# Kernel tuning notes

Measured on AMD Instinct MI355X. Metric: run time of the kernel, lower is better.

## Reference

```python
import jax, jax.numpy as jnp
import numpy as np

B_, T_, L_, M_, H_, F_ = 16, 2048, 128, 256, 512, 1024
EPS = 1e-5


def _init_reservoir(h, rng):
    # orthogonal matrix scaled inside the unit disk for a stable linear recurrence
    q, _ = np.linalg.qr(rng.standard_normal((h, h)).astype(np.float32))
    return jnp.asarray(0.95 * q, dtype=jnp.float32)


def setup_inputs() -> dict:
    key = jax.random.key(0)
    ks = jax.random.split(key, 8)
    rng = np.random.default_rng(0)
    s = lambda fan_in: 1.0 / np.sqrt(fan_in)
    return {
        "x": jax.random.normal(ks[0], (B_, T_, L_), dtype=jnp.float32),
        "We": jax.random.uniform(ks[1], (L_, M_), jnp.float32, -s(L_), s(L_)),
        "be": jnp.zeros((M_,), jnp.float32),
        "Wb": jax.random.uniform(ks[2], (M_, H_), jnp.float32, -s(M_), s(M_)),
        "A": _init_reservoir(H_, rng),
        "Wr": jax.random.uniform(ks[3], (L_, H_), jnp.float32, -s(L_), s(L_)),
        "br": jnp.zeros((H_,), jnp.float32),
        "ln_g": jnp.ones((H_,), jnp.float32),
        "ln_b": jnp.zeros((H_,), jnp.float32),
        "W1": jax.random.uniform(ks[4], (H_, F_), jnp.float32, -s(H_), s(H_)),
        "b1": jnp.zeros((F_,), jnp.float32),
        "W2": jax.random.uniform(ks[5], (F_, H_), jnp.float32, -s(F_), s(F_)),
        "b2": jnp.zeros((H_,), jnp.float32),
    }


def reference(x, We, be, Wb, A, Wr, br, ln_g, ln_b, W1, b1, W2, b2):
    # encoder + B projection, batched over all timesteps: [B,T,H]
    Bu = (x @ We + be) @ Wb

    # sequential linear recurrence h_t = h_{t-1} @ A + Bu_t, h_0 = Bu_0
    def step(h, bu_t):
        h = h @ A + bu_t
        return h, h

    h0 = jnp.zeros((x.shape[0], A.shape[0]), x.dtype)
    _, Hs = jax.lax.scan(step, h0, jnp.swapaxes(Bu, 0, 1))  # [T,B,H]
    H_seq = jnp.swapaxes(Hs, 0, 1)  # [B,T,H]

    # residual + layer norm
    z = H_seq + (x @ Wr + br)
    mu = jnp.mean(z, axis=-1, keepdims=True)
    var = jnp.mean(jnp.square(z - mu), axis=-1, keepdims=True)
    zn = (z - mu) * jax.lax.rsqrt(var + EPS) * ln_g + ln_b

    # MLP on last timestep
    h_last = zn[:, -1, :]
    out = jax.nn.relu(h_last @ W1 + b1) @ W2 + b2
    return out
```

## Files before the change

### kernel.cpp

```cpp
#include <hip/hip_runtime.h>

#define B_  16
#define T_  2048
#define L_  128
#define M_  256
#define H_  512
#define F_  1024
#define EPS 1e-5f

#define LDA_S 36
#define LDB_S 68
#define SMSZ (64 * LDA_S + 64 * LDB_S)

__device__ __forceinline__ float4 load_a4(const float* __restrict__ A,
                                          const float* __restrict__ Alast,
                                          int M, int lda, int amode,
                                          int gr, int gk) {
    float4 av = make_float4(0.f, 0.f, 0.f, 0.f);
    if (gr < M) {
        const float* p;
        if (amode == 1)
            p = A + (long)((gr & 15) * T_ + (T_ - 1 - (gr >> 4))) * L_ + gk;
        else if (amode == 2)
            p = A + (long)(((gr >> 4) << 5) + 16 + (gr & 15)) * lda + gk;
        else if (amode == 3 && gr == M - 1)
            p = Alast + gk;
        else
            p = A + (long)gr * lda + gk;
        av = *(const float4*)p;
    }
    return av;
}

__device__ __forceinline__ void gemm_tile(
    float* sm,
    const float* __restrict__ A, const float* __restrict__ Alast,
    const float* __restrict__ Bm, const float* __restrict__ bias,
    const float* __restrict__ Add, float* __restrict__ C,
    int M, int K, int lda, int ldb, int ldc,
    int flags, int amode, int bx, int by)
{
    constexpr int BM = 32, BN = 64, BK = 64, TM = 2, TN = 4;
    float* As = sm;
    float* Bs = sm + BK * LDA_S;
    const int tid = threadIdx.x;
    const int tx = tid & 15;
    const int ty = tid >> 4;
    const int row0 = by * BM, col0 = bx * BN;

    float4 pa[2], pb[4];
#pragma unroll
    for (int t = 0; t < 2; ++t) {
        int f = tid + t * 256;
        pa[t] = load_a4(A, Alast, M, lda, amode, row0 + (f >> 4), (f & 15) * 4);
    }
#pragma unroll
    for (int t = 0; t < 4; ++t) {
        int f = tid + t * 256;
        pb[t] = *(const float4*)(Bm + (long)(f >> 4) * ldb + col0 + (f & 15) * 4);
    }

    float acc[TM][TN] = {};

    for (int k0 = 0; k0 < K; k0 += BK) {
        __syncthreads();
#pragma unroll
        for (int t = 0; t < 2; ++t) {
            int f = tid + t * 256;
            int arow = f >> 4, kk = (f & 15) * 4;
            As[(kk + 0) * LDA_S + arow] = pa[t].x;
            As[(kk + 1) * LDA_S + arow] = pa[t].y;
            As[(kk + 2) * LDA_S + arow] = pa[t].z;
            As[(kk + 3) * LDA_S + arow] = pa[t].w;
        }
#pragma unroll
        for (int t = 0; t < 4; ++t) {
            int f = tid + t * 256;
            *(float4*)&Bs[(f >> 4) * LDB_S + (f & 15) * 4] = pb[t];
        }
        __syncthreads();
        int kn = k0 + BK;
        if (kn < K) {
#pragma unroll
            for (int t = 0; t < 2; ++t) {
                int f = tid + t * 256;
                pa[t] = load_a4(A, Alast, M, lda, amode, row0 + (f >> 4), kn + (f & 15) * 4);
            }
#pragma unroll
            for (int t = 0; t < 4; ++t) {
                int f = tid + t * 256;
                pb[t] = *(const float4*)(Bm + (long)(kn + (f >> 4)) * ldb + col0 + (f & 15) * 4);
            }
        }
#pragma unroll
        for (int kk = 0; kk < BK; ++kk) {
            float ra[TM], rb[TN];
#pragma unroll
            for (int i = 0; i < TM; ++i) ra[i] = As[kk * LDA_S + ty * TM + i];
#pragma unroll
            for (int j = 0; j < TN; ++j) rb[j] = Bs[kk * LDB_S + tx * TN + j];
#pragma unroll
            for (int i = 0; i < TM; ++i)
#pragma unroll
                for (int j = 0; j < TN; ++j)
                    acc[i][j] = fmaf(ra[i], rb[j], acc[i][j]);
        }
    }

#pragma unroll
    for (int i = 0; i < TM; ++i) {
        int r = row0 + ty * TM + i;
        if (r >= M) continue;
#pragma unroll
        for (int j = 0; j < TN; ++j) {
            int c = col0 + tx * TN + j;
            float v = acc[i][j];
            if (flags & 1) v += bias[c];
            if (amode == 2) v += Add[(long)(((r >> 4) << 5) + (r & 15)) * ldc + c];
            C[(long)r * ldc + c] = v;
        }
    }
}

__global__ __launch_bounds__(256) void dual(
    const float* A, const float* Alast, const float* Bm, const float* bias,
    const float* Add, float* C, int M, int K, int lda, int ldb, int ldc,
    int flags, int amode, int nbxA, int nA,
    const float* SqL, const float* SqR, float* SqOut)
{
    __shared__ float sm[SMSZ];
    int j = blockIdx.x;
    if (j < nA)
        gemm_tile(sm, A, Alast, Bm, bias, Add, C, M, K, lda, ldb, ldc,
                  flags, amode, j % nbxA, j / nbxA);
    else {
        int s = j - nA;
        gemm_tile(sm, SqL, nullptr, SqR, nullptr, nullptr, SqOut,
                  H_, H_, H_, H_, H_, 0, 0, s % 8, s / 8);
    }
}

#define TLDA 20
#define TLDB 68
#define TSM (64 * TLDA + 64 * TLDB)

template <int MODE>
__device__ __forceinline__ float4 tail_a4(const float* __restrict__ Asrc,
                                          const float* __restrict__ x,
                                          int b, int gk) {
    if (MODE == 0) {
        int seg = gk >> 9;
        if (seg < 3)
            return *(const float4*)(Asrc + (long)((seg + 1) * 16 + b) * H_ + (gk & 511));
        return *(const float4*)(x + ((long)b * T_ + (T_ - 1)) * L_ + (gk - 1536));
    } else if (MODE == 1) {
        return *(const float4*)(Asrc + (long)b * H_ + gk);
    } else {
        return *(const float4*)(Asrc + (long)b * F_ + gk);
    }
}

template <int MODE>
__device__ __forceinline__ float4 tail_b4(const float* __restrict__ P32,
                                          const float* __restrict__ P64,
                                          const float* __restrict__ P96,
                                          const float* __restrict__ WrB,
                                          int kr, int c) {
    if (MODE == 0) {
        const float* p;
        if (kr < 512)       p = P32 + (long)kr * H_;
        else if (kr < 1024) p = P64 + (long)(kr - 512) * H_;
        else if (kr < 1536) p = P96 + (long)(kr - 1024) * H_;
        else                p = WrB + (long)(kr - 1536) * H_;
        return *(const float4*)(p + c);
    } else if (MODE == 1) {
        return *(const float4*)(WrB + (long)kr * F_ + c);
    } else {
        return *(const float4*)(WrB + (long)kr * H_ + c);
    }
}

template <int MODE>
__global__ __launch_bounds__(256) void tailgemm(
    const float* __restrict__ Asrc, const float* __restrict__ x,
    const float* __restrict__ P32, const float* __restrict__ P64,
    const float* __restrict__ P96, const float* __restrict__ WrB,
    float* __restrict__ parts, int nbx, int kLen)
{
    constexpr int LDC = (MODE == 1) ? F_ : H_;
    __shared__ float sm[TSM];
    float* As = sm;
    float* Bs = sm + 64 * TLDA;
    const int tid = threadIdx.x;
    const int tx = tid & 15, ty = tid >> 4;
    const int kc = blockIdx.x / nbx;
    const int col0 = (blockIdx.x % nbx) * 64;
    const int kOff = kc * kLen;

    float4 pa, pb[4];
    {
        int gk = kOff + (tid & 15) * 4;
        pa = tail_a4<MODE>(Asrc, x, tid >> 4, gk);
#pragma unroll
        for (int t = 0; t < 4; ++t) {
            int f = tid + t * 256;
            pb[t] = tail_b4<MODE>(P32, P64, P96, WrB, kOff + (f >> 4), col0 + (f & 15) * 4);
        }
    }

    float acc[4] = {};
    for (int k0 = kOff; k0 < kOff + kLen; k0 += 64) {
        __syncthreads();
        {
            int arow = tid >> 4, kk = (tid & 15) * 4;
            As[(kk + 0) * TLDA + arow] = pa.x;
            As[(kk + 1) * TLDA + arow] = pa.y;
            As[(kk + 2) * TLDA + arow] = pa.z;
            As[(kk + 3) * TLDA + arow] = pa.w;
        }
#pragma unroll
        for (int t = 0; t < 4; ++t) {
            int f = tid + t * 256;
            *(float4*)&Bs[(f >> 4) * TLDB + (f & 15) * 4] = pb[t];
        }
        __syncthreads();
        int kn = k0 + 64;
        if (kn < kOff + kLen) {
            pa = tail_a4<MODE>(Asrc, x, tid >> 4, kn + (tid & 15) * 4);
#pragma unroll
            for (int t = 0; t < 4; ++t) {
                int f = tid + t * 256;
                pb[t] = tail_b4<MODE>(P32, P64, P96, WrB, kn + (f >> 4), col0 + (f & 15) * 4);
            }
        }
#pragma unroll
        for (int kk = 0; kk < 64; ++kk) {
            float ra = As[kk * TLDA + ty];
            float4 rb = *(float4*)&Bs[kk * TLDB + tx * 4];
            acc[0] = fmaf(ra, rb.x, acc[0]);
            acc[1] = fmaf(ra, rb.y, acc[1]);
            acc[2] = fmaf(ra, rb.z, acc[2]);
            acc[3] = fmaf(ra, rb.w, acc[3]);
        }
    }

    float* dst = parts + (long)kc * 16 * LDC + (long)ty * LDC + col0 + tx * 4;
    *(float4*)dst = make_float4(acc[0], acc[1], acc[2], acc[3]);
}

__global__ __launch_bounds__(256) void zlnred(
    const float* __restrict__ V1, const float* __restrict__ zparts,
    const float* __restrict__ br, const float* __restrict__ lng,
    const float* __restrict__ lnb, float* __restrict__ zn)
{
    __shared__ float red1[4], red2[4];
    const int b = blockIdx.x, tid = threadIdx.x;
    float z[2];
#pragma unroll
    for (int jj = 0; jj < 2; ++jj) {
        int c = tid + jj * 256;
        float s = V1[(long)b * H_ + c] + br[c];
#pragma unroll
        for (int kc = 0; kc < 13; ++kc)
            s += zparts[(long)kc * 16 * H_ + (long)b * H_ + c];
        z[jj] = s;
    }
    float s1 = z[0] + z[1];
    float s2 = z[0] * z[0] + z[1] * z[1];
#pragma unroll
    for (int off = 32; off > 0; off >>= 1) {
        s1 += __shfl_down(s1, off, 64);
        s2 += __shfl_down(s2, off, 64);
    }
    int wid = tid >> 6, lane = tid & 63;
    if (lane == 0) { red1[wid] = s1; red2[wid] = s2; }
    __syncthreads();
    float S1 = red1[0] + red1[1] + red1[2] + red1[3];
    float S2 = red2[0] + red2[1] + red2[2] + red2[3];
    float mu  = S1 * (1.0f / H_);
    float var = S2 * (1.0f / H_) - mu * mu;
    float rs  = rsqrtf(var + EPS);
#pragma unroll
    for (int jj = 0; jj < 2; ++jj) {
        int c = tid + jj * 256;
        zn[(long)b * H_ + c] = (z[jj] - mu) * rs * lng[c] + lnb[c];
    }
}

__global__ __launch_bounds__(256) void hred(
    const float* __restrict__ h1p, const float* __restrict__ b1,
    float* __restrict__ hid)
{
    int b = blockIdx.x >> 2;
    int c = (blockIdx.x & 3) * 256 + threadIdx.x;
    float s = b1[c];
#pragma unroll
    for (int kc = 0; kc < 4; ++kc)
        s += h1p[(long)kc * 16 * F_ + (long)b * F_ + c];
    hid[(long)b * F_ + c] = fmaxf(s, 0.f);
}

__global__ __launch_bounds__(256) void ored(
    const float* __restrict__ op, const float* __restrict__ b2,
    float* __restrict__ out)
{
    int b = blockIdx.x >> 1;
    int c = (blockIdx.x & 1) * 256 + threadIdx.x;
    float s = b2[c];
#pragma unroll
    for (int kc = 0; kc < 8; ++kc)
        s += op[(long)kc * 16 * H_ + (long)b * H_ + c];
    out[(long)b * H_ + c] = s;
}

extern "C" void kernel_launch(void* const* d_in, const int* in_sizes, int n_in,
                              void* d_out, int out_size, void* d_ws, size_t ws_size,
                              hipStream_t stream) {
    const float* x    = (const float*)d_in[0];
    const float* We   = (const float*)d_in[1];
    const float* be   = (const float*)d_in[2];
    const float* Wb   = (const float*)d_in[3];
    const float* Amat = (const float*)d_in[4];
    const float* Wr   = (const float*)d_in[5];
    const float* br   = (const float*)d_in[6];
    const float* lng  = (const float*)d_in[7];
    const float* lnb  = (const float*)d_in[8];
    const float* W1   = (const float*)d_in[9];
    const float* b1   = (const float*)d_in[10];
    const float* W2   = (const float*)d_in[11];
    const float* b2   = (const float*)d_in[12];
    float* out = (float*)d_out;

    float* ws  = (float*)d_ws;
    float* Wc  = ws;
    float* V0  = Wc + 129 * H_;
    float* V1  = V0 + 2048 * H_;
    float* P2  = V1 + 1024 * H_;
    float* P4  = P2 + H_ * H_;
    float* P8  = P4 + H_ * H_;
    float* P16 = P8 + H_ * H_;
    float* P32 = P16 + H_ * H_;
    float* P64 = P32 + H_ * H_;
    float* P96 = P64 + H_ * H_;
    float* zn  = P96 + H_ * H_;
    float* hid = zn + B_ * H_;
    float* zp  = hid + B_ * F_;
    float* h1p = zp + 13 * B_ * H_;
    float* op  = h1p + 4 * B_ * F_;

    dual<<<168, 256, 0, stream>>>(We, be, Wb, nullptr, nullptr, Wc,
                                  129, M_, M_, H_, H_, 0, 3, 8, 40,
                                  Amat, Amat, P2);
    dual<<<640, 256, 0, stream>>>(x, nullptr, Wc, Wc + 128 * H_, nullptr, V0,
                                  2048, L_, L_, H_, H_, 1, 1, 8, 512,
                                  P2, P2, P4);
    dual<<<384, 256, 0, stream>>>(V0, nullptr, Amat, nullptr, V0, V1,
                                  1024, H_, H_, H_, H_, 0, 2, 8, 256,
                                  P4, P4, P8);
    dual<<<256, 256, 0, stream>>>(V1, nullptr, P2, nullptr, V1, V0,
                                  512, H_, H_, H_, H_, 0, 2, 8, 128,
                                  P8, P8, P16);
    dual<<<192, 256, 0, stream>>>(V0, nullptr, P4, nullptr, V0, V1,
                                  256, H_, H_, H_, H_, 0, 2, 8, 64,
                                  P16, P16, P32);
    dual<<<160, 256, 0, stream>>>(V1, nullptr, P8, nullptr, V1, V0,
                                  128, H_, H_, H_, H_, 0, 2, 8, 32,
                                  P32, P32, P64);
    dual<<<144, 256, 0, stream>>>(V0, nullptr, P16, nullptr, V0, V1,
                                  64, H_, H_, H_, H_, 0, 2, 8, 16,
                                  P32, P64, P96);
    tailgemm<0><<<104, 256, 0, stream>>>(V1, x, P32, P64, P96, Wr, zp, 8, 128);
    zlnred<<<16, 256, 0, stream>>>(V1, zp, br, lng, lnb, zn);
    tailgemm<1><<<64, 256, 0, stream>>>(zn, nullptr, nullptr, nullptr, nullptr,
                                        W1, h1p, 16, 128);
    hred<<<64, 256, 0, stream>>>(h1p, b1, hid);
    tailgemm<2><<<64, 256, 0, stream>>>(hid, nullptr, nullptr, nullptr, nullptr,
                                        W2, op, 8, 128);
    ored<<<32, 256, 0, stream>>>(op, b2, out);
}
```

Before: 284.8 us.

## Use 128x128 split-K GEMM tiles with atomic accumulation and drop reduction kernels

Replaces the 32x64 GEMM tiles in the scan-doubling stages with 128x128 tiles using 8x8 per-thread micro-tiles, splitting K into 128-chunks whose partials are combined with atomicAdd. The tail GEMMs also accumulate atomically, and the hred/ored reduction kernels are removed, with bias and ReLU folded into the A-load of the last GEMM. The aim is more register reuse per loaded element and fewer launches. In exchange it adds a zeroing kernel over the whole workspace and the output, atomic traffic, nondeterministic summation order, and fewer blocks in the small stages.

```diff
diff --git a/kernel.cpp b/kernel.cpp
--- a/kernel.cpp
+++ b/kernel.cpp
@@ -8,135 +8,124 @@
 #define F_  1024
 #define EPS 1e-5f
 
-#define LDA_S 36
-#define LDB_S 68
-#define SMSZ (64 * LDA_S + 64 * LDB_S)
-
-__device__ __forceinline__ float4 load_a4(const float* __restrict__ A,
-                                          const float* __restrict__ Alast,
-                                          int M, int lda, int amode,
-                                          int gr, int gk) {
-    float4 av = make_float4(0.f, 0.f, 0.f, 0.f);
-    if (gr < M) {
-        const float* p;
-        if (amode == 1)
-            p = A + (long)((gr & 15) * T_ + (T_ - 1 - (gr >> 4))) * L_ + gk;
-        else if (amode == 2)
-            p = A + (long)(((gr >> 4) << 5) + 16 + (gr & 15)) * lda + gk;
-        else if (amode == 3 && gr == M - 1)
-            p = Alast + gk;
-        else
-            p = A + (long)gr * lda + gk;
-        av = *(const float4*)p;
-    }
-    return av;
-}
-
-__device__ __forceinline__ void gemm_tile(
+#define LDS_P 132
+#define SM128 (32 * LDS_P * 2)
+
+__device__ __forceinline__ float4 a_load(const float* __restrict__ A,
+                                         const float* __restrict__ Aaux,
+                                         int M, int lda, int amode,
+                                         int gr, int gk) {
+    if (gr >= M) return make_float4(0.f, 0.f, 0.f, 0.f);
+    const float* p;
+    if (amode == 1)
+        p = A + (long)((gr & 15) * T_ + (T_ - 1 - (gr >> 4))) * L_ + gk;
+    else if (amode == 2)
+        p = A + (long)(((gr >> 4) << 5) + 16 + (gr & 15)) * lda + gk;
+    else if (amode == 3 && gr == M - 1)
+        p = Aaux + gk;
+    else
+        p = A + (long)gr * lda + gk;
+    return *(const float4*)p;
+}
+
+__device__ __forceinline__ void gemm128(
     float* sm,
-    const float* __restrict__ A, const float* __restrict__ Alast,
-    const float* __restrict__ Bm, const float* __restrict__ bias,
+    const float* __restrict__ A, const float* __restrict__ Aaux,
+    const float* __restrict__ B, const float* __restrict__ bias,
     const float* __restrict__ Add, float* __restrict__ C,
-    int M, int K, int lda, int ldb, int ldc,
-    int flags, int amode, int bx, int by)
-{
-    constexpr int BM = 32, BN = 64, BK = 64, TM = 2, TN = 4;
+    int M, int lda, int kOff, int kLen, int amode, int kc, int bx, int by)
+{
     float* As = sm;
-    float* Bs = sm + BK * LDA_S;
+    float* Bs = sm + 32 * LDS_P;
     const int tid = threadIdx.x;
-    const int tx = tid & 15;
-    const int ty = tid >> 4;
-    const int row0 = by * BM, col0 = bx * BN;
-
-    float4 pa[2], pb[4];
-#pragma unroll
-    for (int t = 0; t < 2; ++t) {
-        int f = tid + t * 256;
-        pa[t] = load_a4(A, Alast, M, lda, amode, row0 + (f >> 4), (f & 15) * 4);
-    }
+    const int tx = tid & 15, ty = tid >> 4;
+    const int row0 = by * 128, col0 = bx * 128;
+
+    float4 pa[4], pb[4];
 #pragma unroll
     for (int t = 0; t < 4; ++t) {
         int f = tid + t * 256;
-        pb[t] = *(const float4*)(Bm + (long)(f >> 4) * ldb + col0 + (f & 15) * 4);
-    }
-
-    float acc[TM][TN] = {};
-
-    for (int k0 = 0; k0 < K; k0 += BK) {
+        pa[t] = a_load(A, Aaux, M, lda, amode, row0 + (f >> 3), kOff + (f & 7) * 4);
+        pb[t] = *(const float4*)(B + (long)(kOff + (f >> 5)) * H_ + col0 + (f & 31) * 4);
+    }
+
+    float acc[8][8] = {};
+
+    for (int k0 = 0; k0 < kLen; k0 += 32) {
         __syncthreads();
-#pragma unroll
-        for (int t = 0; t < 2; ++t) {
-            int f = tid + t * 256;
-            int arow = f >> 4, kk = (f & 15) * 4;
-            As[(kk + 0) * LDA_S + arow] = pa[t].x;
-            As[(kk + 1) * LDA_S + arow] = pa[t].y;
-            As[(kk + 2) * LDA_S + arow] = pa[t].z;
-            As[(kk + 3) * LDA_S + arow] = pa[t].w;
-        }
 #pragma unroll
         for (int t = 0; t < 4; ++t) {
             int f = tid + t * 256;
-            *(float4*)&Bs[(f >> 4) * LDB_S + (f & 15) * 4] = pb[t];
+            int ar = f >> 3, ak = (f & 7) * 4;
+            As[(ak + 0) * LDS_P + ar] = pa[t].x;
+            As[(ak + 1) * LDS_P + ar] = pa[t].y;
+            As[(ak + 2) * LDS_P + ar] = pa[t].z;
+            As[(ak + 3) * LDS_P + ar] = pa[t].w;
+            *(float4*)&Bs[(f >> 5) * LDS_P + (f & 31) * 4] = pb[t];
         }
         __syncthreads();
-        int kn = k0 + BK;
-        if (kn < K) {
-#pragma unroll
-            for (int t = 0; t < 2; ++t) {
-                int f = tid + t * 256;
-                pa[t] = load_a4(A, Alast, M, lda, amode, row0 + (f >> 4), kn + (f & 15) * 4);
-            }
+        int kn = k0 + 32;
+        if (kn < kLen) {
 #pragma unroll
             for (int t = 0; t < 4; ++t) {
                 int f = tid + t * 256;
-                pb[t] = *(const float4*)(Bm + (long)(kn + (f >> 4)) * ldb + col0 + (f & 15) * 4);
+                pa[t] = a_load(A, Aaux, M, lda, amode, row0 + (f >> 3),
+                               kOff + kn + (f & 7) * 4);
+                pb[t] = *(const float4*)(B + (long)(kOff + kn + (f >> 5)) * H_ +
+                                         col0 + (f & 31) * 4);
             }
         }
 #pragma unroll
-        for (int kk = 0; kk < BK; ++kk) {
-            float ra[TM], rb[TN];
-#pragma unroll
-            for (int i = 0; i < TM; ++i) ra[i] = As[kk * LDA_S + ty * TM + i];
-#pragma unroll
-            for (int j = 0; j < TN; ++j) rb[j] = Bs[kk * LDB_S + tx * TN + j];
-#pragma unroll
-            for (int i = 0; i < TM; ++i)
-#pragma unroll
-                for (int j = 0; j < TN; ++j)
+        for (int kk = 0; kk < 32; ++kk) {
+            float ra[8], rb[8];
+#pragma unroll
+            for (int i = 0; i < 8; ++i) ra[i] = As[kk * LDS_P + ty * 8 + i];
+#pragma unroll
+            for (int j = 0; j < 8; ++j) rb[j] = Bs[kk * LDS_P + tx * 8 + j];
+#pragma unroll
+            for (int i = 0; i < 8; ++i)
+#pragma unroll
+                for (int j = 0; j < 8; ++j)
                     acc[i][j] = fmaf(ra[i], rb[j], acc[i][j]);
         }
     }
 
 #pragma unroll
-    for (int i = 0; i < TM; ++i) {
-        int r = row0 + ty * TM + i;
+    for (int i = 0; i < 8; ++i) {
+        int r = row0 + ty * 8 + i;
         if (r >= M) continue;
-#pragma unroll
-        for (int j = 0; j < TN; ++j) {
-            int c = col0 + tx * TN + j;
+        long addoff = (amode == 2) ? (long)(((r >> 4) << 5) + (r & 15)) * H_ : 0;
+#pragma unroll
+        for (int j = 0; j < 8; ++j) {
+            int c = col0 + tx * 8 + j;
             float v = acc[i][j];
-            if (flags & 1) v += bias[c];
-            if (amode == 2) v += Add[(long)(((r >> 4) << 5) + (r & 15)) * ldc + c];
-            C[(long)r * ldc + c] = v;
-        }
-    }
-}
-
-__global__ __launch_bounds__(256) void dual(
-    const float* A, const float* Alast, const float* Bm, const float* bias,
-    const float* Add, float* C, int M, int K, int lda, int ldb, int ldc,
-    int flags, int amode, int nbxA, int nA,
-    const float* SqL, const float* SqR, float* SqOut)
-{
-    __shared__ float sm[SMSZ];
+            if (kc == 0 && bias) v += bias[c];
+            if (kc == 0 && Add)  v += Add[addoff + c];
+            atomicAdd(&C[(long)r * H_ + c], v);
+        }
+    }
+}
+
+__global__ __launch_bounds__(256) void dual128(
+    const float* A, const float* Aaux, const float* B, const float* bias,
+    const float* Add, float* C, int M, int lda, int kLen,
+    int nbxA, int nrtA, int amode, int nA,
+    const float* PL, const float* PR, float* PO)
+{
+    __shared__ float sm[SM128];
     int j = blockIdx.x;
-    if (j < nA)
-        gemm_tile(sm, A, Alast, Bm, bias, Add, C, M, K, lda, ldb, ldc,
-                  flags, amode, j % nbxA, j / nbxA);
-    else {
+    if (j < nA) {
+        int bx = j % nbxA;
+        int r  = j / nbxA;
+        int by = r % nrtA;
+        int kc = r / nrtA;
+        gemm128(sm, A, Aaux, B, bias, Add, C, M, lda, kc * kLen, kLen,
+                amode, kc, bx, by);
+    } else {
         int s = j - nA;
-        gemm_tile(sm, SqL, nullptr, SqR, nullptr, nullptr, SqOut,
-                  H_, H_, H_, H_, H_, 0, 0, s % 8, s / 8);
+        int bx = s & 3, by = (s >> 2) & 3, kc = s >> 4;
+        gemm128(sm, PL, nullptr, PR, nullptr, nullptr, PO, 512, 512,
+                kc * 128, 128, 0, kc, bx, by);
     }
 }
 
@@ -146,17 +135,20 @@
 
 template <int MODE>
 __device__ __forceinline__ float4 tail_a4(const float* __restrict__ Asrc,
-                                          const float* __restrict__ x,
+                                          const float* __restrict__ aux,
                                           int b, int gk) {
     if (MODE == 0) {
         int seg = gk >> 9;
         if (seg < 3)
             return *(const float4*)(Asrc + (long)((seg + 1) * 16 + b) * H_ + (gk & 511));
-        return *(const float4*)(x + ((long)b * T_ + (T_ - 1)) * L_ + (gk - 1536));
+        return *(const float4*)(aux + ((long)b * T_ + (T_ - 1)) * L_ + (gk - 1536));
     } else if (MODE == 1) {
         return *(const float4*)(Asrc + (long)b * H_ + gk);
     } else {
-        return *(const float4*)(Asrc + (long)b * F_ + gk);
+        float4 h = *(const float4*)(Asrc + (long)b * F_ + gk);
+        float4 bb = *(const float4*)(aux + gk);
+        return make_float4(fmaxf(h.x + bb.x, 0.f), fmaxf(h.y + bb.y, 0.f),
+                           fmaxf(h.z + bb.z, 0.f), fmaxf(h.w + bb.w, 0.f));
     }
 }
 
@@ -164,28 +156,29 @@
 __device__ __forceinline__ float4 tail_b4(const float* __restrict__ P32,
                                           const float* __restrict__ P64,
                                           const float* __restrict__ P96,
-                                          const float* __restrict__ WrB,
+                                          const float* __restrict__ WB,
                                           int kr, int c) {
     if (MODE == 0) {
         const float* p;
         if (kr < 512)       p = P32 + (long)kr * H_;
         else if (kr < 1024) p = P64 + (long)(kr - 512) * H_;
         else if (kr < 1536) p = P96 + (long)(kr - 1024) * H_;
-        else                p = WrB + (long)(kr - 1536) * H_;
+        else                p = WB + (long)(kr - 1536) * H_;
         return *(const float4*)(p + c);
     } else if (MODE == 1) {
-        return *(const float4*)(WrB + (long)kr * F_ + c);
+        return *(const float4*)(WB + (long)kr * F_ + c);
     } else {
-        return *(const float4*)(WrB + (long)kr * H_ + c);
+        return *(const float4*)(WB + (long)kr * H_ + c);
     }
 }
 
 template <int MODE>
 __global__ __launch_bounds__(256) void tailgemm(
-    const float* __restrict__ Asrc, const float* __restrict__ x,
+    const float* __restrict__ Asrc, const float* __restrict__ aux,
     const float* __restrict__ P32, const float* __restrict__ P64,
-    const float* __restrict__ P96, const float* __restrict__ WrB,
-    float* __restrict__ parts, int nbx, int kLen)
+    const float* __restrict__ P96, const float* __restrict__ WB,
+    const float* __restrict__ bias2, float* __restrict__ Cacc,
+    int nbx, int kLen)
 {
     constexpr int LDC = (MODE == 1) ? F_ : H_;
     __shared__ float sm[TSM];
@@ -198,25 +191,22 @@
     const int kOff = kc * kLen;
 
     float4 pa, pb[4];
-    {
-        int gk = kOff + (tid & 15) * 4;
-        pa = tail_a4<MODE>(Asrc, x, tid >> 4, gk);
-#pragma unroll
-        for (int t = 0; t < 4; ++t) {
-            int f = tid + t * 256;
-            pb[t] = tail_b4<MODE>(P32, P64, P96, WrB, kOff + (f >> 4), col0 + (f & 15) * 4);
-        }
+    pa = tail_a4<MODE>(Asrc, aux, ty, kOff + tx * 4);
+#pragma unroll
+    for (int t = 0; t < 4; ++t) {
+        int f = tid + t * 256;
+        pb[t] = tail_b4<MODE>(P32, P64, P96, WB, kOff + (f >> 4), col0 + (f & 15) * 4);
     }
 
     float acc[4] = {};
-    for (int k0 = kOff; k0 < kOff + kLen; k0 += 64) {
+    for (int k0 = 0; k0 < kLen; k0 += 64) {
         __syncthreads();
         {
-            int arow = tid >> 4, kk = (tid & 15) * 4;
-            As[(kk + 0) * TLDA + arow] = pa.x;
-            As[(kk + 1) * TLDA + arow] = pa.y;
-            As[(kk + 2) * TLDA + arow] = pa.z;
-            As[(kk + 3) * TLDA + arow] = pa.w;
+            int kk = tx * 4;
+            As[(kk + 0) * TLDA + ty] = pa.x;
+            As[(kk + 1) * TLDA + ty] = pa.y;
+            As[(kk + 2) * TLDA + ty] = pa.z;
+            As[(kk + 3) * TLDA + ty] = pa.w;
         }
 #pragma unroll
         for (int t = 0; t < 4; ++t) {
@@ -225,12 +215,13 @@
         }
         __syncthreads();
         int kn = k0 + 64;
-        if (kn < kOff + kLen) {
-            pa = tail_a4<MODE>(Asrc, x, tid >> 4, kn + (tid & 15) * 4);
+        if (kn < kLen) {
+            pa = tail_a4<MODE>(Asrc, aux, ty, kOff + kn + tx * 4);
 #pragma unroll
             for (int t = 0; t < 4; ++t) {
                 int f = tid + t * 256;
-                pb[t] = tail_b4<MODE>(P32, P64, P96, WrB, kn + (f >> 4), col0 + (f & 15) * 4);
+                pb[t] = tail_b4<MODE>(P32, P64, P96, WB, kOff + kn + (f >> 4),
+                                      col0 + (f & 15) * 4);
             }
         }
 #pragma unroll
@@ -244,12 +235,17 @@
         }
     }
 
-    float* dst = parts + (long)kc * 16 * LDC + (long)ty * LDC + col0 + tx * 4;
-    *(float4*)dst = make_float4(acc[0], acc[1], acc[2], acc[3]);
+    float* dst = Cacc + (long)ty * LDC + col0 + tx * 4;
+#pragma unroll
+    for (int q = 0; q < 4; ++q) {
+        float v = acc[q];
+        if (MODE == 2 && kc == 0 && bias2) v += bias2[col0 + tx * 4 + q];
+        atomicAdd(dst + q, v);
+    }
 }
 
 __global__ __launch_bounds__(256) void zlnred(
-    const float* __restrict__ V1, const float* __restrict__ zparts,
+    const float* __restrict__ Y5, const float* __restrict__ zacc,
     const float* __restrict__ br, const float* __restrict__ lng,
     const float* __restrict__ lnb, float* __restrict__ zn)
 {
@@ -259,11 +255,7 @@
 #pragma unroll
     for (int jj = 0; jj < 2; ++jj) {
         int c = tid + jj * 256;
-        float s = V1[(long)b * H_ + c] + br[c];
-#pragma unroll
-        for (int kc = 0; kc < 13; ++kc)
-            s += zparts[(long)kc * 16 * H_ + (long)b * H_ + c];
-        z[jj] = s;
+        z[jj] = Y5[(long)b * H_ + c] + zacc[(long)b * H_ + c] + br[c];
     }
     float s1 = z[0] + z[1];
     float s2 = z[0] * z[0] + z[1] * z[1];
@@ -287,30 +279,13 @@
     }
 }
 
-__global__ __launch_bounds__(256) void hred(
-    const float* __restrict__ h1p, const float* __restrict__ b1,
-    float* __restrict__ hid)
-{
-    int b = blockIdx.x >> 2;
-    int c = (blockIdx.x & 3) * 256 + threadIdx.x;
-    float s = b1[c];
-#pragma unroll
-    for (int kc = 0; kc < 4; ++kc)
-        s += h1p[(long)kc * 16 * F_ + (long)b * F_ + c];
-    hid[(long)b * F_ + c] = fmaxf(s, 0.f);
-}
-
-__global__ __launch_bounds__(256) void ored(
-    const float* __restrict__ op, const float* __restrict__ b2,
-    float* __restrict__ out)
-{
-    int b = blockIdx.x >> 1;
-    int c = (blockIdx.x & 1) * 256 + threadIdx.x;
-    float s = b2[c];
-#pragma unroll
-    for (int kc = 0; kc < 8; ++kc)
-        s += op[(long)kc * 16 * H_ + (long)b * H_ + c];
-    out[(long)b * H_ + c] = s;
+__global__ __launch_bounds__(256) void zerok(float4* w, long n4, float4* o, long n4o)
+{
+    long stride = (long)gridDim.x * 256;
+    for (long i = (long)blockIdx.x * 256 + threadIdx.x; i < n4; i += stride)
+        w[i] = make_float4(0.f, 0.f, 0.f, 0.f);
+    for (long i = (long)blockIdx.x * 256 + threadIdx.x; i < n4o; i += stride)
+        o[i] = make_float4(0.f, 0.f, 0.f, 0.f);
 }
 
 extern "C" void kernel_launch(void* const* d_in, const int* in_sizes, int n_in,
@@ -331,50 +306,47 @@
     const float* b2   = (const float*)d_in[12];
     float* out = (float*)d_out;
 
-    float* ws  = (float*)d_ws;
-    float* Wc  = ws;
-    float* V0  = Wc + 129 * H_;
-    float* V1  = V0 + 2048 * H_;
-    float* P2  = V1 + 1024 * H_;
-    float* P4  = P2 + H_ * H_;
-    float* P8  = P4 + H_ * H_;
-    float* P16 = P8 + H_ * H_;
-    float* P32 = P16 + H_ * H_;
-    float* P64 = P32 + H_ * H_;
-    float* P96 = P64 + H_ * H_;
-    float* zn  = P96 + H_ * H_;
-    float* hid = zn + B_ * H_;
-    float* zp  = hid + B_ * F_;
-    float* h1p = zp + 13 * B_ * H_;
-    float* op  = h1p + 4 * B_ * F_;
-
-    dual<<<168, 256, 0, stream>>>(We, be, Wb, nullptr, nullptr, Wc,
-                                  129, M_, M_, H_, H_, 0, 3, 8, 40,
-                                  Amat, Amat, P2);
-    dual<<<640, 256, 0, stream>>>(x, nullptr, Wc, Wc + 128 * H_, nullptr, V0,
-                                  2048, L_, L_, H_, H_, 1, 1, 8, 512,
-                                  P2, P2, P4);
-    dual<<<384, 256, 0, stream>>>(V0, nullptr, Amat, nullptr, V0, V1,
-                                  1024, H_, H_, H_, H_, 0, 2, 8, 256,
-                                  P4, P4, P8);
-    dual<<<256, 256, 0, stream>>>(V1, nullptr, P2, nullptr, V1, V0,
-                                  512, H_, H_, H_, H_, 0, 2, 8, 128,
-                                  P8, P8, P16);
-    dual<<<192, 256, 0, stream>>>(V0, nullptr, P4, nullptr, V0, V1,
-                                  256, H_, H_, H_, H_, 0, 2, 8, 64,
-                                  P16, P16, P32);
-    dual<<<160, 256, 0, stream>>>(V1, nullptr, P8, nullptr, V1, V0,
-                                  128, H_, H_, H_, H_, 0, 2, 8, 32,
-                                  P32, P32, P64);
-    dual<<<144, 256, 0, stream>>>(V0, nullptr, P16, nullptr, V0, V1,
-                                  64, H_, H_, H_, H_, 0, 2, 8, 16,
-                                  P32, P64, P96);
-    tailgemm<0><<<104, 256, 0, stream>>>(V1, x, P32, P64, P96, Wr, zp, 8, 128);
-    zlnred<<<16, 256, 0, stream>>>(V1, zp, br, lng, lnb, zn);
+    float* ws   = (float*)d_ws;
+    float* Wc   = ws;
+    float* P2   = Wc + 129 * H_;
+    float* P4   = P2 + H_ * H_;
+    float* P8   = P4 + H_ * H_;
+    float* P16  = P8 + H_ * H_;
+    float* P32  = P16 + H_ * H_;
+    float* P64  = P32 + H_ * H_;
+    float* P96  = P64 + H_ * H_;
+    float* Y1   = P96 + H_ * H_;
+    float* Y2   = Y1 + 1024 * H_;
+    float* Y3   = Y2 + 512 * H_;
+    float* Y4   = Y3 + 256 * H_;
+    float* Y5   = Y4 + 128 * H_;
+    float* zacc = Y5 + 64 * H_;
+    float* hacc = zacc + B_ * H_;
+    float* U0   = hacc + B_ * F_;
+    float* zn   = U0 + 2048 * H_;
+    long zeroN = (long)(zn - ws);
+
+    zerok<<<1024, 256, 0, stream>>>((float4*)ws, zeroN / 4, (float4*)out,
+                                    (long)out_size / 4);
+    dual128<<<80, 256, 0, stream>>>(We, be, Wb, nullptr, nullptr, Wc,
+                                    129, M_, 128, 4, 2, 3, 16, Amat, Amat, P2);
+    dual128<<<128, 256, 0, stream>>>(x, nullptr, Wc, Wc + 128 * H_, nullptr, U0,
+                                     2048, 0, 128, 4, 16, 1, 64, P2, P2, P4);
+    dual128<<<192, 256, 0, stream>>>(U0, nullptr, Amat, nullptr, U0, Y1,
+                                     1024, H_, 128, 4, 8, 2, 128, P4, P4, P8);
+    dual128<<<128, 256, 0, stream>>>(Y1, nullptr, P2, nullptr, Y1, Y2,
+                                     512, H_, 128, 4, 4, 2, 64, P8, P8, P16);
+    dual128<<<96, 256, 0, stream>>>(Y2, nullptr, P4, nullptr, Y2, Y3,
+                                    256, H_, 128, 4, 2, 2, 32, P16, P16, P32);
+    dual128<<<80, 256, 0, stream>>>(Y3, nullptr, P8, nullptr, Y3, Y4,
+                                    128, H_, 128, 4, 1, 2, 16, P32, P32, P64);
+    dual128<<<80, 256, 0, stream>>>(Y4, nullptr, P16, nullptr, Y4, Y5,
+                                    64, H_, 128, 4, 1, 2, 16, P32, P64, P96);
+    tailgemm<0><<<104, 256, 0, stream>>>(Y5, x, P32, P64, P96, Wr, nullptr,
+                                         zacc, 8, 128);
+    zlnred<<<16, 256, 0, stream>>>(Y5, zacc, br, lng, lnb, zn);
     tailgemm<1><<<64, 256, 0, stream>>>(zn, nullptr, nullptr, nullptr, nullptr,
-                                        W1, h1p, 16, 128);
-    hred<<<64, 256, 0, stream>>>(h1p, b1, hid);
-    tailgemm<2><<<64, 256, 0, stream>>>(hid, nullptr, nullptr, nullptr, nullptr,
-                                        W2, op, 8, 128);
-    ored<<<32, 256, 0, stream>>>(op, b2, out);
-}
+                                        W1, nullptr, hacc, 16, 128);
+    tailgemm<2><<<64, 256, 0, stream>>>(hacc, b1, nullptr, nullptr, nullptr,
+                                        W2, b2, out, 8, 128);
+}
```

Result: slower. 820.1 us (+187.9%).
